# Kernel tuning notes

Hardware: AMD Instinct MI355X
Metric: run time of the kernel (lower is better)

The kernel has to match this reference:

```python
import jax, jax.numpy as jnp
import numpy as np

N = 8192
D = 256
E = 131072


def setup_inputs() -> dict:
    key = jax.random.key(0)
    k1, k2 = jax.random.split(key)
    l_enc = jax.random.normal(k1, (N, D), dtype=jnp.float32)
    edge_index = jax.random.randint(k2, (2, E), 0, N, dtype=jnp.int64)
    return {"l_enc": l_enc, "edge_index": edge_index}


def reference(l_enc, edge_index):
    n = l_enc.shape[0]
    dt = l_enc.dtype
    # Vectorized symmetric adjacency build (replaces the per-edge Python loop).
    adj = (
        jnp.zeros((n, n), dtype=dt)
        .at[edge_index[0], edge_index[1]].set(1.0)
        .at[edge_index[1], edge_index[0]].set(1.0)
    )
    # Dense Gram matrix + sigmoid, diagonal zeroed like (1 - eye) * res.
    res = jax.nn.sigmoid(jnp.matmul(l_enc, l_enc.T))
    mask = jnp.eye(n, dtype=dt)
    res = (1.0 - mask) * res
    # BCE with torch-style log clamp at -100 (handles res == 0 on the diagonal).
    log_p = jnp.maximum(jnp.log(res), -100.0)
    log_1mp = jnp.maximum(jnp.log1p(-res), -100.0)
    return jnp.mean(-(adj * log_p + (1.0 - adj) * log_1mp))
```

## Files before the change

### kernel.cpp

```cpp
#include <hip/hip_runtime.h>
#include <hip/hip_bf16.h>

#define NN 8192
#define DK 256
#define NE 131072
#define T128 64
#define NBLK (T128*(T128+1)/2)

typedef __attribute__((ext_vector_type(8))) short bf16x8;
typedef __attribute__((ext_vector_type(4))) float f32x4;
typedef const __attribute__((address_space(1))) void* gas1_t;
typedef __attribute__((address_space(3))) void* las3_t;

__device__ __align__(16) unsigned       g_mask[(size_t)NN*NN/32];
__device__ __align__(16) unsigned short g_bf[(size_t)NN*DK];
__device__ __align__(16) double g_part[NBLK];

__device__ __forceinline__ unsigned short f2bf(float f) {
    unsigned u = __float_as_uint(f);
    unsigned r = (u + 0x7FFFu + ((u >> 16) & 1u)) >> 16;
    return (unsigned short)r;
}

__global__ void k_prep(const float* __restrict__ x) {
    int i = blockIdx.x * 256 + threadIdx.x;
    uint4 z; z.x = z.y = z.z = z.w = 0u;
    *(uint4*)(&g_mask[(size_t)i * 4]) = z;
    float4 v = ((const float4*)x)[i];
    ushort4 b;
    b.x = f2bf(v.x); b.y = f2bf(v.y); b.z = f2bf(v.z); b.w = f2bf(v.w);
    *(ushort4*)(&g_bf[(size_t)i * 4]) = b;
}

__global__ void k_scatter(const long long* __restrict__ ei) {
    int e = blockIdx.x * 256 + threadIdx.x;
    if (e >= NE) return;
    int i = (int)ei[e];
    int j = (int)ei[NE + e];
    atomicOr(&g_mask[(size_t)i * (NN/32) + (j >> 5)], 1u << (j & 31));
    atomicOr(&g_mask[(size_t)j * (NN/32) + (i >> 5)], 1u << (i & 31));
}

__global__ __launch_bounds__(256, 3) void k_loss() {
    __shared__ __align__(16) unsigned short lsA[128 * 64];
    __shared__ __align__(16) unsigned short lsB[128 * 64];
    __shared__ double s_part[4];

    int orig = blockIdx.x;
    int bid  = (orig & 7) * (NBLK / 8) + (orig >> 3);
    int rem = bid, ti = 0;
    while (rem >= T128 - ti) { rem -= T128 - ti; ++ti; }
    int tj = ti + rem;

    const int tid  = threadIdx.x;
    const int lane = tid & 63;
    const int w    = tid >> 6;
    const int wr   = w >> 1;
    const int wc   = w & 1;
    const int lr   = lane & 15;
    const int lq   = lane >> 4;

    const int gq = (tid & 7) ^ ((tid >> 3) & 7);
    const unsigned short* srcA0 = g_bf + (size_t)(ti * 128 + (tid >> 3)) * DK + gq * 8;
    const size_t dB = (size_t)(tj - ti) * 128 * DK;
    const int lds0 = tid * 8;

#define STAGE(kt) do {                                                             \
    _Pragma("unroll")                                                              \
    for (int i = 0; i < 4; ++i) {                                                  \
        __builtin_amdgcn_global_load_lds(                                          \
            (gas1_t)(const void*)(srcA0 + (size_t)i * 32 * DK + (kt) * 64),        \
            (las3_t)(void*)&lsA[lds0 + i * 2048], 16, 0, 0);                       \
        __builtin_amdgcn_global_load_lds(                                          \
            (gas1_t)(const void*)(srcA0 + dB + (size_t)i * 32 * DK + (kt) * 64),   \
            (las3_t)(void*)&lsB[lds0 + i * 2048], 16, 0, 0);                       \
    }                                                                              \
} while (0)

    f32x4 acc[4][4] = {};

    STAGE(0);
    __syncthreads();

    #pragma unroll
    for (int kt = 0; kt < 4; ++kt) {
        #pragma unroll
        for (int ks = 0; ks < 2; ++ks) {
            const int cq = (ks * 4 + lq) ^ (lr & 7);
            bf16x8 fa[4];
            #pragma unroll
            for (int fm = 0; fm < 4; ++fm) {
                int ra = wr * 64 + fm * 16 + lr;
                fa[fm] = *(const bf16x8*)((const char*)&lsA[0] + ra * 128 + cq * 16);
            }
            #pragma unroll
            for (int fn = 0; fn < 4; ++fn) {
                int rb = wc * 64 + fn * 16 + lr;
                bf16x8 fbv = *(const bf16x8*)((const char*)&lsB[0] + rb * 128 + cq * 16);
                #pragma unroll
                for (int fm = 0; fm < 4; ++fm)
                    acc[fm][fn] = __builtin_amdgcn_mfma_f32_16x16x32_bf16(
                        fa[fm], fbv, acc[fm][fn], 0, 0, 0);
            }
        }
        if (kt < 3) {
            __syncthreads();
            STAGE(kt + 1);
            __syncthreads();
        }
    }
#undef STAGE

    const int R0 = ti * 128 + wr * 64;
    const int C0 = tj * 128 + wc * 64;
    const char* mrow0 = (const char*)g_mask + (size_t)(C0 >> 5) * 4;
    const bool diagB = (ti == tj) && (wr == wc);
    float tsum = 0.0f;
    #pragma unroll
    for (int fm = 0; fm < 4; ++fm) {
        #pragma unroll
        for (int r2 = 0; r2 < 4; ++r2) {
            int rowg = R0 + fm * 16 + lq * 4 + r2;
            uint2 m2 = *(const uint2*)(mrow0 + (size_t)rowg * (NN / 8));
            #pragma unroll
            for (int fn = 0; fn < 4; ++fn) {
                float s = acc[fm][fn][r2];
                unsigned mw = (fn & 2) ? m2.y : m2.x;
                int bit = (mw >> ((fn & 1) * 16 + lr)) & 1;
                float u   = fmaxf(s * 1.44269504f, -126.0f);
                float e   = __builtin_amdgcn_exp2f(-u);
                float opE = 1.0f + e;
                float lE  = __builtin_amdgcn_logf(opE);
                float t1  = 0.6931471805599453f * lE;
                bool  sat = (opE == 1.0f);
                bool  ovf = (s < -88.722839f);
                float term0 = sat ? 100.0f : fmaxf(t1 + s, 0.0f);
                float term1 = ovf ? 100.0f : t1;
                float term  = bit ? term1 : term0;
                if (diagB && fm == fn && (lq * 4 + r2) == lr)
                    term = bit ? 100.0f : 0.0f;
                tsum += term;
            }
        }
    }
    #pragma unroll
    for (int off = 32; off; off >>= 1) tsum += __shfl_down(tsum, off);
    if (lane == 0) {
        float wgt = (ti == tj) ? 1.0f : 2.0f;
        s_part[w] = (double)(tsum * wgt);
    }
    __syncthreads();
    if (tid == 0)
        g_part[orig] = (s_part[0] + s_part[1]) + (s_part[2] + s_part[3]);
}

__global__ void k_final(float* __restrict__ out) {
    __shared__ double sd[256];
    double s = 0.0;
    for (int i = threadIdx.x; i < NBLK; i += 256) s += g_part[i];
    sd[threadIdx.x] = s;
    __syncthreads();
    #pragma unroll
    for (int st = 128; st; st >>= 1) {
        if (threadIdx.x < st) sd[threadIdx.x] += sd[threadIdx.x + st];
        __syncthreads();
    }
    if (threadIdx.x == 0)
        out[0] = (float)(sd[0] * (1.0 / ((double)NN * (double)NN)));
}

extern "C" void kernel_launch(void* const* d_in, const int* in_sizes, int n_in,
                              void* d_out, int out_size, void* d_ws, size_t ws_size,
                              hipStream_t stream) {
    const float* l_enc = (const float*)d_in[0];
    const long long* ei = (const long long*)d_in[1];
    float* out = (float*)d_out;

    k_prep<<<2048, 256, 0, stream>>>(l_enc);
    k_scatter<<<NE / 256, 256, 0, stream>>>(ei);
    k_loss<<<NBLK, 256, 0, stream>>>();
    k_final<<<1, 256, 0, stream>>>(out);
}
```

Baseline: 60.30 us.

## Fuse final reduction into loss kernel via last-block atomic, simplify BCE epilogue

Drops the separate k_final launch. Each loss block bumps a global counter after writing its partial, and the last block to finish reduces all partials and writes the output. Separately, the per-element BCE epilogue becomes a single softplus form: the sign is flipped by the edge bit, and a threshold compare replaces the saturation/overflow checks. This saves one kernel launch and a few ALU ops per element, at the cost of an atomic and fences per block plus a serial tail reduction.

```diff
diff --git a/kernel.cpp b/kernel.cpp
--- a/kernel.cpp
+++ b/kernel.cpp
@@ -15,6 +15,7 @@
 __device__ __align__(16) unsigned       g_mask[(size_t)NN*NN/32];
 __device__ __align__(16) unsigned short g_bf[(size_t)NN*DK];
 __device__ __align__(16) double g_part[NBLK];
+__device__ unsigned g_done;
 
 __device__ __forceinline__ unsigned short f2bf(float f) {
     unsigned u = __float_as_uint(f);
@@ -30,6 +31,7 @@
     ushort4 b;
     b.x = f2bf(v.x); b.y = f2bf(v.y); b.z = f2bf(v.z); b.w = f2bf(v.w);
     *(ushort4*)(&g_bf[(size_t)i * 4]) = b;
+    if (i == 0) g_done = 0u;
 }
 
 __global__ void k_scatter(const long long* __restrict__ ei) {
@@ -41,10 +43,11 @@
     atomicOr(&g_mask[(size_t)j * (NN/32) + (i >> 5)], 1u << (i & 31));
 }
 
-__global__ __launch_bounds__(256, 3) void k_loss() {
+__global__ __launch_bounds__(256, 3) void k_loss(float* __restrict__ out) {
     __shared__ __align__(16) unsigned short lsA[128 * 64];
     __shared__ __align__(16) unsigned short lsB[128 * 64];
     __shared__ double s_part[4];
+    __shared__ int s_fin;
 
     int orig = blockIdx.x;
     int bid  = (orig & 7) * (NBLK / 8) + (orig >> 3);
@@ -126,17 +129,13 @@
             for (int fn = 0; fn < 4; ++fn) {
                 float s = acc[fm][fn][r2];
                 unsigned mw = (fn & 2) ? m2.y : m2.x;
-                int bit = (mw >> ((fn & 1) * 16 + lr)) & 1;
-                float u   = fmaxf(s * 1.44269504f, -126.0f);
-                float e   = __builtin_amdgcn_exp2f(-u);
-                float opE = 1.0f + e;
-                float lE  = __builtin_amdgcn_logf(opE);
-                float t1  = 0.6931471805599453f * lE;
-                bool  sat = (opE == 1.0f);
-                bool  ovf = (s < -88.722839f);
-                float term0 = sat ? 100.0f : fmaxf(t1 + s, 0.0f);
-                float term1 = ovf ? 100.0f : t1;
-                float term  = bit ? term1 : term0;
+                bool bit = ((mw >> ((fn & 1) * 16 + lr)) & 1) != 0;
+                float x  = bit ? -s : s;
+                float wv = x * 1.44269504f;
+                float e2 = __builtin_amdgcn_exp2f(fminf(wv, 126.0f));
+                float t  = 0.6931471805599453f * __builtin_amdgcn_logf(1.0f + e2);
+                float thr = bit ? 128.0f : 24.0f;
+                float term = (wv >= thr) ? 100.0f : t;
                 if (diagB && fm == fn && (lq * 4 + r2) == lr)
                     term = bit ? 100.0f : 0.0f;
                 tsum += term;
@@ -150,23 +149,29 @@
         s_part[w] = (double)(tsum * wgt);
     }
     __syncthreads();
-    if (tid == 0)
+    if (tid == 0) {
         g_part[orig] = (s_part[0] + s_part[1]) + (s_part[2] + s_part[3]);
-}
+        __threadfence();
+        unsigned t = atomicAdd(&g_done, 1u);
+        s_fin = (t == NBLK - 1u) ? 1 : 0;
+    }
+    __syncthreads();
 
-__global__ void k_final(float* __restrict__ out) {
-    __shared__ double sd[256];
-    double s = 0.0;
-    for (int i = threadIdx.x; i < NBLK; i += 256) s += g_part[i];
-    sd[threadIdx.x] = s;
-    __syncthreads();
-    #pragma unroll
-    for (int st = 128; st; st >>= 1) {
-        if (threadIdx.x < st) sd[threadIdx.x] += sd[threadIdx.x + st];
+    if (s_fin) {
+        __threadfence();
+        double* sd = (double*)lsA;
+        double sacc = 0.0;
+        for (int i = tid; i < NBLK; i += 256) sacc += g_part[i];
+        sd[tid] = sacc;
         __syncthreads();
+        #pragma unroll
+        for (int st = 128; st; st >>= 1) {
+            if (tid < st) sd[tid] += sd[tid + st];
+            __syncthreads();
+        }
+        if (tid == 0)
+            out[0] = (float)(sd[0] * (1.0 / ((double)NN * (double)NN)));
     }
-    if (threadIdx.x == 0)
-        out[0] = (float)(sd[0] * (1.0 / ((double)NN * (double)NN)));
 }
 
 extern "C" void kernel_launch(void* const* d_in, const int* in_sizes, int n_in,
@@ -178,6 +183,5 @@
 
     k_prep<<<2048, 256, 0, stream>>>(l_enc);
     k_scatter<<<NE / 256, 256, 0, stream>>>(ei);
-    k_loss<<<NBLK, 256, 0, stream>>>();
-    k_final<<<1, 256, 0, stream>>>(out);
+    k_loss<<<NBLK, 256, 0, stream>>>(out);
 }
```

After: 108.0 us. 1.79x slower.
